# Optimization experiments

Hardware: AMD Instinct MI355X
Metric: run time of the kernel (lower is better)

Reference implementation:

```python
import jax, jax.numpy as jnp
import numpy as np

B, F, NUM_LAYERS, T, DEPTH, C = 256, 128, 4, 2048, 6, 100
L = 2 ** DEPTH  # num_leaves = 64

# bit pattern of the oblivious tree: bit d of leaf_idx (MSB-first),
# matching (leaf_idx // (L >> (d+1))) % 2 in the original double loop
_BITS = np.stack([(np.arange(L) // (L >> (d + 1))) % 2 for d in range(DEPTH)])  # [DEPTH, L]


def setup_inputs() -> dict:
    key = jax.random.key(0)
    k = jax.random.split(key, 5)
    x = jax.random.normal(k[0], (B, F), dtype=jnp.float32)
    sel_W = jax.random.normal(k[1], (NUM_LAYERS, T * DEPTH, F), dtype=jnp.float32) * 0.05
    sel_b = jax.random.normal(k[2], (NUM_LAYERS, T * DEPTH), dtype=jnp.float32) * 0.01
    out_W = jax.random.normal(k[3], (C, NUM_LAYERS * T * L), dtype=jnp.float32) * 0.002
    out_b = jax.random.normal(k[4], (C,), dtype=jnp.float32) * 0.01
    return {"x": x, "sel_W": sel_W, "sel_b": sel_b, "out_W": out_W, "out_b": out_b}


def reference(x, sel_W, sel_b, out_W, out_b):
    bits = jnp.asarray(_BITS, dtype=x.dtype)  # [DEPTH, L]
    layer_outputs = []
    for i in range(NUM_LAYERS):
        # feature selector linear -> [B, T, DEPTH] threshold responses
        fv = jax.nn.sigmoid(x @ sel_W[i].T + sel_b[i]).reshape(B, T, DEPTH)
        # leaf probability = prod over depth of (left or right prob per bit)
        leaf = jnp.ones((B, T, L), dtype=x.dtype)
        for d in range(DEPTH):  # fixed small structural loop (depth=6)
            p = fv[:, :, d:d + 1]                     # [B, T, 1] left prob
            bit = bits[d]                             # [L]
            leaf = leaf * (p * (1.0 - bit) + (1.0 - p) * bit)
        layer_outputs.append(leaf.reshape(B, T * L))
    combined = jnp.concatenate(layer_outputs, axis=1)  # [B, NUM_LAYERS*T*L]
    return combined @ out_W.T + out_b
```

## Files before the change

### kernel.cpp

```cpp
#include <hip/hip_runtime.h>
#include <hip/hip_bf16.h>

#define BB 256
#define FF 128
#define CC 100
#define KG 512
#define ITPB 16
#define NIT 8192
#define WT_IT 7168

typedef short bf16x8 __attribute__((ext_vector_type(8)));
typedef float f32x4 __attribute__((ext_vector_type(4)));
typedef _Float16 f16x8 __attribute__((ext_vector_type(8)));

static __device__ inline unsigned short f2bf(float f) {
    unsigned u = __float_as_uint(f);
    u += 0x7fffu + ((u >> 16) & 1u);
    return (unsigned short)(u >> 16);
}
static __device__ inline float bf2f(unsigned short h) {
    return __uint_as_float(((unsigned)h) << 16);
}
static __device__ inline unsigned pk2(float a, float b) {
    __hip_bfloat162 h = __float22bfloat162_rn(float2{a, b});
    union { __hip_bfloat162 h2; unsigned u; } cv; cv.h2 = h;
    return cv.u;
}

__global__ __launch_bounds__(256) void fv_kernel(
    const float* __restrict__ x, const float* __restrict__ selW,
    const float* __restrict__ selb, unsigned short* __restrict__ fvout)
{
    __shared__ unsigned short wt[128 * 136];
    __shared__ unsigned short xt[128 * 136];
    __shared__ float sb[128];

    const int tid = threadIdx.x;
    const int m0 = blockIdx.x * 128;
    const int n0 = blockIdx.y * 128;

    #pragma unroll 4
    for (int pass = 0; pass < 16; ++pass) {
        int idx = pass * 256 + tid;
        int r = idx >> 5, f4 = idx & 31;
        float4 v = *((const float4*)(selW + (size_t)(m0 + r) * FF) + f4);
        float4 vx = *((const float4*)(x + (size_t)(n0 + r) * FF) + f4);
        ushort4 h;
        h.x = f2bf(v.x); h.y = f2bf(v.y); h.z = f2bf(v.z); h.w = f2bf(v.w);
        *(ushort4*)(wt + r * 136 + f4 * 4) = h;
        ushort4 hx;
        hx.x = f2bf(vx.x); hx.y = f2bf(vx.y); hx.z = f2bf(vx.z); hx.w = f2bf(vx.w);
        *(ushort4*)(xt + r * 136 + f4 * 4) = hx;
    }
    if (tid < 128) sb[tid] = selb[m0 + tid];
    __syncthreads();

    const int w = tid >> 6, lane = tid & 63;
    const int q = lane >> 4, l15 = lane & 15;
    const int mq = w & 1, nq = w >> 1;

    f32x4 zero4 = {0.f, 0.f, 0.f, 0.f};
    f32x4 acc[4][4];
    #pragma unroll
    for (int i = 0; i < 4; ++i)
        #pragma unroll
        for (int j = 0; j < 4; ++j) acc[i][j] = zero4;

    #pragma unroll
    for (int ch = 0; ch < 4; ++ch) {
        bf16x8 a[4];
        #pragma unroll
        for (int ms = 0; ms < 4; ++ms)
            a[ms] = *(const bf16x8*)(wt + (mq * 64 + ms * 16 + l15) * 136 + ch * 32 + q * 8);
        #pragma unroll
        for (int ns = 0; ns < 4; ++ns) {
            bf16x8 bfr = *(const bf16x8*)(xt + (nq * 64 + ns * 16 + l15) * 136 + ch * 32 + q * 8);
            #pragma unroll
            for (int ms = 0; ms < 4; ++ms)
                acc[ms][ns] = __builtin_amdgcn_mfma_f32_16x16x32_bf16(a[ms], bfr, acc[ms][ns], 0, 0, 0);
        }
    }

    #pragma unroll
    for (int ms = 0; ms < 4; ++ms) {
        int rowl = mq * 64 + ms * 16 + q * 4;
        #pragma unroll
        for (int ns = 0; ns < 4; ++ns) {
            int b = n0 + nq * 64 + ns * 16 + l15;
            #pragma unroll
            for (int reg = 0; reg < 4; ++reg) {
                int row = m0 + rowl + reg;
                float z = acc[ms][ns][reg] + sb[rowl + reg];
                float p = 1.0f / (1.0f + __expf(-z));
                fvout[(size_t)row * 256 + b] = f2bf(p);
            }
        }
    }
}

__global__ __launch_bounds__(256) void wt_kernel(
    const float* __restrict__ outW, unsigned short* __restrict__ Wt)
{
    __shared__ unsigned short tile[WT_IT];
    const int tid = threadIdx.x;
    const int it = blockIdx.x;

    #pragma unroll
    for (int i = 0; i < 4; ++i) {
        int s = i * 256 + tid;
        if (s < 896) *(uint4*)(tile + s * 8) = make_uint4(0, 0, 0, 0);
    }
    __syncthreads();

    const int cr = tid >> 4;
    const int f4 = tid & 15;
    const int ch4 = (f4 >> 3) * 4 + ((f4 >> 1) & 3);
    const int j0 = (f4 & 1) * 4;

    float4 v[7];
    #pragma unroll
    for (int pass = 0; pass < 7; ++pass) {
        const int c = pass * 16 + cr;
        v[pass] = make_float4(0.f, 0.f, 0.f, 0.f);
        if (c < CC)
            v[pass] = *((const float4*)(outW + (size_t)c * 524288 + (size_t)it * 64) + f4);
    }
    #pragma unroll
    for (int pass = 0; pass < 7; ++pass) {
        const int c = pass * 16 + cr;
        if (c < CC) {
            unsigned lo = pk2(v[pass].x, v[pass].y);
            unsigned hi = pk2(v[pass].z, v[pass].w);
            *(uint2*)(tile + (ch4 * 112 + c) * 8 + j0) = make_uint2(lo, hi);
        }
    }
    __syncthreads();

    uint4* dst = (uint4*)(Wt + (size_t)it * WT_IT);
    const uint4* src = (const uint4*)tile;
    #pragma unroll
    for (int i = 0; i < 4; ++i) {
        int s = i * 256 + tid;
        if (s < 896) dst[s] = src[s];
    }
}

__global__ __launch_bounds__(256, 2) void main_gemm(
    const unsigned short* __restrict__ fv, const unsigned short* __restrict__ Wt,
    _Float16* __restrict__ part16)
{
    const int tid = threadIdx.x;
    const int kg = blockIdx.x;
    const int w = tid >> 6, lane = tid & 63;
    const int q = lane >> 4, l15 = lane & 15;
    const int qh = q >> 1, ql = q & 1;

    f32x4 zero4 = {0.f, 0.f, 0.f, 0.f};
    f32x4 acc[4][7];
    #pragma unroll
    for (int i = 0; i < 4; ++i)
        #pragma unroll
        for (int j = 0; j < 7; ++j) acc[i][j] = zero4;

    unsigned short pvb[2][6];
    {
        const unsigned short* fp = fv + (size_t)(kg * ITPB) * 1536 + tid;
        #pragma unroll
        for (int d = 0; d < 6; ++d) pvb[0][d] = fp[d * 256];
    }

    for (int itl = 0; itl < ITPB; ++itl) {
        const int it = kg * ITPB + itl;
        const int cur = itl & 1;

        if (itl + 1 < ITPB) {
            const unsigned short* fp = fv + (size_t)(it + 1) * 1536 + tid;
            #pragma unroll
            for (int d = 0; d < 6; ++d) pvb[cur ^ 1][d] = fp[d * 256];
        }

        const unsigned short* wbase = Wt + (size_t)it * WT_IT;
        bf16x8 bfr[2][7];
        #pragma unroll
        for (int ch = 0; ch < 2; ++ch)
            #pragma unroll
            for (int nt = 0; nt < 7; ++nt)
                bfr[ch][nt] = *(const bf16x8*)(wbase + ((ch * 4 + q) * 112 + nt * 16 + l15) * 8);

        float p[6];
        #pragma unroll
        for (int d = 0; d < 6; ++d) p[d] = bf2f(pvb[cur][d]);

        bf16x8 afr[4][2];
        #pragma unroll
        for (int ms = 0; ms < 4; ++ms) {
            const int src = ms * 16 + l15;
            float s0 = __shfl(p[0], src, 64);
            float s1 = __shfl(p[1], src, 64);
            float s2 = __shfl(p[2], src, 64);
            float s3 = __shfl(p[3], src, 64);
            float s4 = __shfl(p[4], src, 64);
            float s5 = __shfl(p[5], src, 64);
            float t1 = qh ? (1.f - s1) : s1;
            float A0 = s0 * t1;
            float A1 = (1.f - s0) * t1;
            float t2 = ql ? (1.f - s2) : s2;
            float Bv0 = t2 * s3;
            float Bv1 = t2 * (1.f - s3);
            float n4 = 1.f - s4, n5 = 1.f - s5;
            float Cv0 = s4 * s5, Cv1 = s4 * n5, Cv2 = n4 * s5, Cv3 = n4 * n5;
            #pragma unroll
            for (int ch = 0; ch < 2; ++ch) {
                float A = ch ? A1 : A0;
                float ab0 = A * Bv0, ab1 = A * Bv1;
                union { bf16x8 v; unsigned u[4]; } bu;
                bu.u[0] = pk2(ab0 * Cv0, ab0 * Cv1);
                bu.u[1] = pk2(ab0 * Cv2, ab0 * Cv3);
                bu.u[2] = pk2(ab1 * Cv0, ab1 * Cv1);
                bu.u[3] = pk2(ab1 * Cv2, ab1 * Cv3);
                afr[ms][ch] = bu.v;
            }
        }

        #pragma unroll
        for (int ch = 0; ch < 2; ++ch)
            #pragma unroll
            for (int nt = 0; nt < 7; ++nt)
                #pragma unroll
                for (int ms = 0; ms < 4; ++ms)
                    acc[ms][nt] = __builtin_amdgcn_mfma_f32_16x16x32_bf16(
                        afr[ms][ch], bfr[ch][nt], acc[ms][nt], 0, 0, 0);
    }

    #pragma unroll
    for (int ms = 0; ms < 4; ++ms) {
        const int brow = w * 64 + ms * 16 + q * 4;
        #pragma unroll
        for (int nt = 0; nt < 7; ++nt) {
            const int c = nt * 16 + l15;
            #pragma unroll
            for (int reg = 0; reg < 4; ++reg)
                part16[((size_t)(brow + reg) * KG + kg) * 112 + c] =
                    (_Float16)acc[ms][nt][reg];
        }
    }
}

__global__ __launch_bounds__(256) void reduce_k(
    const _Float16* __restrict__ part16, const float* __restrict__ outb,
    float* __restrict__ out)
{
    __shared__ float red[16 * 112];
    const int b = blockIdx.x;
    const int tid = threadIdx.x;
    const f16x8* slice = (const f16x8*)(part16 + (size_t)b * (KG * 112));

    if (tid < 224) {
        const int c8 = tid % 14;
        const int kgs = tid / 14;
        float s[8];
        #pragma unroll
        for (int j = 0; j < 8; ++j) s[j] = 0.f;
        #pragma unroll 4
        for (int i = 0; i < 32; ++i) {
            f16x8 v = slice[i * 224 + tid];
            #pragma unroll
            for (int j = 0; j < 8; ++j) s[j] += (float)v[j];
        }
        #pragma unroll
        for (int j = 0; j < 8; ++j) red[kgs * 112 + c8 * 8 + j] = s[j];
    }
    __syncthreads();
    if (tid < CC) {
        float r = outb[tid];
        #pragma unroll
        for (int k = 0; k < 16; ++k) r += red[k * 112 + tid];
        out[b * CC + tid] = r;
    }
}

extern "C" void kernel_launch(void* const* d_in, const int* in_sizes, int n_in,
                              void* d_out, int out_size, void* d_ws, size_t ws_size,
                              hipStream_t stream) {
    const float* x    = (const float*)d_in[0];
    const float* selW = (const float*)d_in[1];
    const float* selb = (const float*)d_in[2];
    const float* outW = (const float*)d_in[3];
    const float* outb = (const float*)d_in[4];
    float* out = (float*)d_out;

    unsigned short* fv = (unsigned short*)d_ws;
    unsigned short* Wt = (unsigned short*)((char*)d_ws + 25165824);
    _Float16* part16 = (_Float16*)((char*)d_ws + 142606336);

    wt_kernel<<<NIT, 256, 0, stream>>>(outW, Wt);
    fv_kernel<<<dim3(384, 2), 256, 0, stream>>>(x, selW, selb, fv);
    main_gemm<<<KG, 256, 0, stream>>>(fv, Wt, part16);
    reduce_k<<<BB, 256, 0, stream>>>(part16, outb, out);
}
```

Before: 421.3 us.

## Fuse weight transpose into GEMM via direct global-to-LDS fp32 loads

Drops the separate wt_kernel, which converted out_W to a bf16 transposed workspace, and has main_gemm stream fp32 out_W straight into double-buffered LDS using global_load_lds with a swizzled slot layout. Conversion to bf16 now happens when fragments are read from LDS. The grid becomes 256 K-groups by 2 class-halves with fewer accumulators per block, and the reduce loop is shortened to match. This removes a full write and reread of the weight workspace, but the GEMM now reads twice as many bytes in fp32, leans on hand-written waitcnt and barrier sync, and recomputes the leaf products in both class halves.

```diff
diff --git a/kernel.cpp b/kernel.cpp
--- a/kernel.cpp
+++ b/kernel.cpp
@@ -4,10 +4,9 @@
 #define BB 256
 #define FF 128
 #define CC 100
-#define KG 512
-#define ITPB 16
-#define NIT 8192
-#define WT_IT 7168
+#define KG 256
+#define ITPB 32
+#define NMACRO 16
 
 typedef short bf16x8 __attribute__((ext_vector_type(8)));
 typedef float f32x4 __attribute__((ext_vector_type(4)));
@@ -25,6 +24,11 @@
     __hip_bfloat162 h = __float22bfloat162_rn(float2{a, b});
     union { __hip_bfloat162 h2; unsigned u; } cv; cv.h2 = h;
     return cv.u;
+}
+static __device__ inline void gl_lds16(const float* g, float* l) {
+    __builtin_amdgcn_global_load_lds(
+        (const __attribute__((address_space(1))) void*)g,
+        (__attribute__((address_space(3))) void*)l, 16, 0, 0);
 }
 
 __global__ __launch_bounds__(256) void fv_kernel(
@@ -98,152 +102,154 @@
     }
 }
 
-__global__ __launch_bounds__(256) void wt_kernel(
-    const float* __restrict__ outW, unsigned short* __restrict__ Wt)
-{
-    __shared__ unsigned short tile[WT_IT];
-    const int tid = threadIdx.x;
-    const int it = blockIdx.x;
-
-    #pragma unroll
-    for (int i = 0; i < 4; ++i) {
-        int s = i * 256 + tid;
-        if (s < 896) *(uint4*)(tile + s * 8) = make_uint4(0, 0, 0, 0);
-    }
-    __syncthreads();
-
-    const int cr = tid >> 4;
-    const int f4 = tid & 15;
-    const int ch4 = (f4 >> 3) * 4 + ((f4 >> 1) & 3);
-    const int j0 = (f4 & 1) * 4;
-
-    float4 v[7];
-    #pragma unroll
-    for (int pass = 0; pass < 7; ++pass) {
-        const int c = pass * 16 + cr;
-        v[pass] = make_float4(0.f, 0.f, 0.f, 0.f);
-        if (c < CC)
-            v[pass] = *((const float4*)(outW + (size_t)c * 524288 + (size_t)it * 64) + f4);
-    }
-    #pragma unroll
-    for (int pass = 0; pass < 7; ++pass) {
-        const int c = pass * 16 + cr;
-        if (c < CC) {
-            unsigned lo = pk2(v[pass].x, v[pass].y);
-            unsigned hi = pk2(v[pass].z, v[pass].w);
-            *(uint2*)(tile + (ch4 * 112 + c) * 8 + j0) = make_uint2(lo, hi);
-        }
-    }
-    __syncthreads();
-
-    uint4* dst = (uint4*)(Wt + (size_t)it * WT_IT);
-    const uint4* src = (const uint4*)tile;
-    #pragma unroll
-    for (int i = 0; i < 4; ++i) {
-        int s = i * 256 + tid;
-        if (s < 896) dst[s] = src[s];
-    }
-}
-
 __global__ __launch_bounds__(256, 2) void main_gemm(
-    const unsigned short* __restrict__ fv, const unsigned short* __restrict__ Wt,
+    const unsigned short* __restrict__ fv, const float* __restrict__ outW,
     _Float16* __restrict__ part16)
 {
+    __shared__ float buf[2][8192];
+
     const int tid = threadIdx.x;
     const int kg = blockIdx.x;
+    const int cg = blockIdx.y;
     const int w = tid >> 6, lane = tid & 63;
     const int q = lane >> 4, l15 = lane & 15;
     const int qh = q >> 1, ql = q & 1;
+    const int cmax = cg ? 43 : 55;
+    const int half = lane >> 5;
 
     f32x4 zero4 = {0.f, 0.f, 0.f, 0.f};
-    f32x4 acc[4][7];
+    f32x4 acc[4][4];
     #pragma unroll
     for (int i = 0; i < 4; ++i)
         #pragma unroll
-        for (int j = 0; j < 7; ++j) acc[i][j] = zero4;
-
-    unsigned short pvb[2][6];
-    {
-        const unsigned short* fp = fv + (size_t)(kg * ITPB) * 1536 + tid;
-        #pragma unroll
-        for (int d = 0; d < 6; ++d) pvb[0][d] = fp[d * 256];
-    }
-
-    for (int itl = 0; itl < ITPB; ++itl) {
-        const int it = kg * ITPB + itl;
-        const int cur = itl & 1;
-
-        if (itl + 1 < ITPB) {
-            const unsigned short* fp = fv + (size_t)(it + 1) * 1536 + tid;
-            #pragma unroll
-            for (int d = 0; d < 6; ++d) pvb[cur ^ 1][d] = fp[d * 256];
-        }
-
-        const unsigned short* wbase = Wt + (size_t)it * WT_IT;
-        bf16x8 bfr[2][7];
-        #pragma unroll
-        for (int ch = 0; ch < 2; ++ch)
-            #pragma unroll
-            for (int nt = 0; nt < 7; ++nt)
-                bfr[ch][nt] = *(const bf16x8*)(wbase + ((ch * 4 + q) * 112 + nt * 16 + l15) * 8);
-
-        float p[6];
-        #pragma unroll
-        for (int d = 0; d < 6; ++d) p[d] = bf2f(pvb[cur][d]);
-
-        bf16x8 afr[4][2];
-        #pragma unroll
-        for (int ms = 0; ms < 4; ++ms) {
-            const int src = ms * 16 + l15;
-            float s0 = __shfl(p[0], src, 64);
-            float s1 = __shfl(p[1], src, 64);
-            float s2 = __shfl(p[2], src, 64);
-            float s3 = __shfl(p[3], src, 64);
-            float s4 = __shfl(p[4], src, 64);
-            float s5 = __shfl(p[5], src, 64);
-            float t1 = qh ? (1.f - s1) : s1;
-            float A0 = s0 * t1;
-            float A1 = (1.f - s0) * t1;
-            float t2 = ql ? (1.f - s2) : s2;
-            float Bv0 = t2 * s3;
-            float Bv1 = t2 * (1.f - s3);
-            float n4 = 1.f - s4, n5 = 1.f - s5;
-            float Cv0 = s4 * s5, Cv1 = s4 * n5, Cv2 = n4 * s5, Cv3 = n4 * n5;
-            #pragma unroll
-            for (int ch = 0; ch < 2; ++ch) {
-                float A = ch ? A1 : A0;
-                float ab0 = A * Bv0, ab1 = A * Bv1;
+        for (int j = 0; j < 4; ++j) acc[i][j] = zero4;
+
+    const unsigned short* fvp = fv + tid;
+    unsigned short fvh[2][12];
+
+    #define ISSUE_GROUP(mm, nb)                                                  \
+    {                                                                            \
+        const size_t g0 = (size_t)kg * 2048 + (size_t)(mm) * 128;                \
+        _Pragma("unroll")                                                        \
+        for (int j = 0; j < 8; ++j) {                                            \
+            const int rbase = w * 16 + 2 * j;                                    \
+            const int r = rbase + half;                                          \
+            const int s = r & 7;                                                 \
+            const int slot = ((lane & 31) + s) & 31;                             \
+            const int rc = r > cmax ? cmax : r;                                  \
+            const int c = cg * 56 + rc;                                          \
+            gl_lds16(outW + (size_t)c * 524288 + g0 + slot * 4,                  \
+                     &buf[nb][rbase * 128]);                                     \
+        }                                                                        \
+        const int it0 = kg * ITPB + (mm) * 2;                                    \
+        _Pragma("unroll")                                                        \
+        for (int e = 0; e < 12; ++e)                                             \
+            fvh[nb][e] = fvp[((size_t)(it0 + (e >= 6 ? 1 : 0)) * 6 + (e % 6)) * 256]; \
+    }
+
+    ISSUE_GROUP(0, 0);
+    ISSUE_GROUP(1, 1);
+
+    #pragma unroll 2
+    for (int m = 0; m < NMACRO; ++m) {
+        const int cur = m & 1;
+
+        asm volatile("s_waitcnt vmcnt(20)\n\ts_barrier" ::: "memory");
+
+        bf16x8 bfr[4][4];
+        #pragma unroll
+        for (int ch = 0; ch < 4; ++ch) {
+            #pragma unroll
+            for (int nt = 0; nt < 4; ++nt) {
+                const int r = nt * 16 + l15;
+                const int s = r & 7;
+                const int sl0 = ((ch * 8 + q * 2) - s) & 31;
+                const int sl1 = ((ch * 8 + q * 2 + 1) - s) & 31;
+                f32x4 lo = *(const f32x4*)&buf[cur][r * 128 + sl0 * 4];
+                f32x4 hi = *(const f32x4*)&buf[cur][r * 128 + sl1 * 4];
                 union { bf16x8 v; unsigned u[4]; } bu;
-                bu.u[0] = pk2(ab0 * Cv0, ab0 * Cv1);
-                bu.u[1] = pk2(ab0 * Cv2, ab0 * Cv3);
-                bu.u[2] = pk2(ab1 * Cv0, ab1 * Cv1);
-                bu.u[3] = pk2(ab1 * Cv2, ab1 * Cv3);
-                afr[ms][ch] = bu.v;
-            }
-        }
-
-        #pragma unroll
-        for (int ch = 0; ch < 2; ++ch)
-            #pragma unroll
-            for (int nt = 0; nt < 7; ++nt)
+                bu.u[0] = pk2(lo[0], lo[1]);
+                bu.u[1] = pk2(lo[2], lo[3]);
+                bu.u[2] = pk2(hi[0], hi[1]);
+                bu.u[3] = pk2(hi[2], hi[3]);
+                bfr[ch][nt] = bu.v;
+            }
+        }
+
+        #pragma unroll
+        for (int itl = 0; itl < 2; ++itl) {
+            float p0 = bf2f(fvh[cur][itl * 6 + 0]);
+            float p1 = bf2f(fvh[cur][itl * 6 + 1]);
+            float p2 = bf2f(fvh[cur][itl * 6 + 2]);
+            float p3 = bf2f(fvh[cur][itl * 6 + 3]);
+            float p4 = bf2f(fvh[cur][itl * 6 + 4]);
+            float p5 = bf2f(fvh[cur][itl * 6 + 5]);
+
+            bf16x8 afr[4][2];
+            #pragma unroll
+            for (int ms = 0; ms < 4; ++ms) {
+                const int src = ms * 16 + l15;
+                float s0 = __shfl(p0, src, 64);
+                float s1 = __shfl(p1, src, 64);
+                float s2 = __shfl(p2, src, 64);
+                float s3 = __shfl(p3, src, 64);
+                float s4 = __shfl(p4, src, 64);
+                float s5 = __shfl(p5, src, 64);
+                float t1 = qh ? (1.f - s1) : s1;
+                float A0 = s0 * t1;
+                float A1 = (1.f - s0) * t1;
+                float t2 = ql ? (1.f - s2) : s2;
+                float Bv0 = t2 * s3;
+                float Bv1 = t2 * (1.f - s3);
+                float n4 = 1.f - s4, n5 = 1.f - s5;
+                float Cv0 = s4 * s5, Cv1 = s4 * n5, Cv2 = n4 * s5, Cv3 = n4 * n5;
                 #pragma unroll
-                for (int ms = 0; ms < 4; ++ms)
-                    acc[ms][nt] = __builtin_amdgcn_mfma_f32_16x16x32_bf16(
-                        afr[ms][ch], bfr[ch][nt], acc[ms][nt], 0, 0, 0);
-    }
-
+                for (int chl = 0; chl < 2; ++chl) {
+                    float A = chl ? A1 : A0;
+                    float ab0 = A * Bv0, ab1 = A * Bv1;
+                    union { bf16x8 v; unsigned u[4]; } bu;
+                    bu.u[0] = pk2(ab0 * Cv0, ab0 * Cv1);
+                    bu.u[1] = pk2(ab0 * Cv2, ab0 * Cv3);
+                    bu.u[2] = pk2(ab1 * Cv0, ab1 * Cv1);
+                    bu.u[3] = pk2(ab1 * Cv2, ab1 * Cv3);
+                    afr[ms][chl] = bu.v;
+                }
+            }
+            #pragma unroll
+            for (int chl = 0; chl < 2; ++chl) {
+                const int ch = itl * 2 + chl;
+                #pragma unroll
+                for (int nt = 0; nt < 4; ++nt)
+                    #pragma unroll
+                    for (int ms = 0; ms < 4; ++ms)
+                        acc[ms][nt] = __builtin_amdgcn_mfma_f32_16x16x32_bf16(
+                            afr[ms][chl], bfr[ch][nt], acc[ms][nt], 0, 0, 0);
+            }
+        }
+
+        asm volatile("s_waitcnt lgkmcnt(0)\n\ts_barrier" ::: "memory");
+
+        const int mn = (m + 2 < NMACRO) ? (m + 2) : m;
+        ISSUE_GROUP(mn, cur);
+    }
+
+    const int slotmax = cg ? 44 : 56;
     #pragma unroll
     for (int ms = 0; ms < 4; ++ms) {
         const int brow = w * 64 + ms * 16 + q * 4;
         #pragma unroll
-        for (int nt = 0; nt < 7; ++nt) {
-            const int c = nt * 16 + l15;
-            #pragma unroll
-            for (int reg = 0; reg < 4; ++reg)
-                part16[((size_t)(brow + reg) * KG + kg) * 112 + c] =
-                    (_Float16)acc[ms][nt][reg];
-        }
-    }
+        for (int nt = 0; nt < 4; ++nt) {
+            const int slot = nt * 16 + l15;
+            if (slot < slotmax) {
+                const int c = cg * 56 + slot;
+                #pragma unroll
+                for (int reg = 0; reg < 4; ++reg)
+                    part16[((size_t)(brow + reg) * KG + kg) * 112 + c] =
+                        (_Float16)acc[ms][nt][reg];
+            }
+        }
+    }
+    #undef ISSUE_GROUP
 }
 
 __global__ __launch_bounds__(256) void reduce_k(
@@ -262,7 +268,7 @@
         #pragma unroll
         for (int j = 0; j < 8; ++j) s[j] = 0.f;
         #pragma unroll 4
-        for (int i = 0; i < 32; ++i) {
+        for (int i = 0; i < 16; ++i) {
             f16x8 v = slice[i * 224 + tid];
             #pragma unroll
             for (int j = 0; j < 8; ++j) s[j] += (float)v[j];
@@ -290,11 +296,9 @@
     float* out = (float*)d_out;
 
     unsigned short* fv = (unsigned short*)d_ws;
-    unsigned short* Wt = (unsigned short*)((char*)d_ws + 25165824);
-    _Float16* part16 = (_Float16*)((char*)d_ws + 142606336);
-
-    wt_kernel<<<NIT, 256, 0, stream>>>(outW, Wt);
+    _Float16* part16 = (_Float16*)((char*)d_ws + 25165824);
+
     fv_kernel<<<dim3(384, 2), 256, 0, stream>>>(x, selW, selb, fv);
-    main_gemm<<<KG, 256, 0, stream>>>(fv, Wt, part16);
+    main_gemm<<<dim3(KG, 2), 256, 0, stream>>>(fv, outW, part16);
     reduce_k<<<BB, 256, 0, stream>>>(part16, outb, out);
 }
```

New measurement: 350.6 us. 1.2x faster.
